# Performance work log

Measured on AMD Instinct MI355X. Metric: run time of the kernel, lower is better.

The kernel has to match this reference:

```python
import jax, jax.numpy as jnp
import numpy as np

N = 50000      # nodes
E = 800000     # edges
C = 128        # in channels
H = 128        # hidden1 = hidden2 = hidden3
B = 256        # graphs in batch
CLS = 10       # classes
MLP_H = 64
EPS = 1e-5


def _lin_params(key, fan_in, fan_out):
    k1, k2 = jax.random.split(key)
    s = 1.0 / np.sqrt(fan_in)
    W = jax.random.uniform(k1, (fan_in, fan_out), jnp.float32, -s, s)
    b = jax.random.uniform(k2, (fan_out,), jnp.float32, -s, s)
    return W, b


def setup_inputs() -> dict:
    key = jax.random.key(0)
    ks = jax.random.split(key, 10)
    x = jax.random.normal(ks[0], (N, C), jnp.float32)
    edge_index = jax.random.randint(ks[1], (2, E), 0, N)
    edge_attr = jax.random.uniform(ks[2], (E,), jnp.float32)
    batch = jnp.sort(jax.random.randint(ks[3], (N,), 0, B))
    W1, b1 = _lin_params(ks[4], C, H)
    W2, b2 = _lin_params(ks[5], H, H)
    W3, b3 = _lin_params(ks[6], H, H)
    gamma = jnp.ones((H,), jnp.float32)
    beta = jnp.zeros((H,), jnp.float32)
    Wm1, bm1 = _lin_params(ks[7], H, MLP_H)
    Wm2, bm2 = _lin_params(ks[8], MLP_H, CLS)
    return dict(x=x, edge_index=edge_index, edge_attr=edge_attr, batch=batch,
                W1=W1, b1=b1, W2=W2, b2=b2, W3=W3, b3=b3,
                gamma=gamma, beta=beta, Wm1=Wm1, bm1=bm1, Wm2=Wm2, bm2=bm2)


def gcn_conv(x, src, dst, ew, W, b):
    # PyG GCNConv: linear (no bias) -> gcn_norm with self-loops -> scatter-add -> +bias
    h = x @ W                                                  # [N, out]
    deg = jax.ops.segment_sum(ew, dst, num_segments=N) + 1.0   # self-loop weight 1
    dinv = jnp.where(deg > 0, jax.lax.rsqrt(deg), 0.0)
    norm = dinv[src] * ew * dinv[dst]                          # [E]
    agg = jax.ops.segment_sum(norm[:, None] * h[src], dst, num_segments=N)
    agg = agg + h * (dinv * dinv)[:, None]                     # self-loop messages
    return agg + b


def reference(x, edge_index, edge_attr, batch,
              W1, b1, W2, b2, W3, b3, gamma, beta, Wm1, bm1, Wm2, bm2):
    src, dst = edge_index[0], edge_index[1]
    ew = edge_attr.reshape(-1)
    h = jax.nn.relu(gcn_conv(x, src, dst, ew, W1, b1))
    h = jax.nn.relu(gcn_conv(h, src, dst, ew, W2, b2))
    h = jax.nn.relu(gcn_conv(h, src, dst, ew, W3, b3))
    # BatchNorm (training-mode batch stats, biased variance)
    mu = jnp.mean(h, axis=0)
    var = jnp.mean((h - mu) ** 2, axis=0)
    h = (h - mu) * jax.lax.rsqrt(var + EPS) * gamma + beta
    # global_mean_pool over graph ids
    counts = jax.ops.segment_sum(jnp.ones((N,), jnp.float32), batch, num_segments=B)
    g = jax.ops.segment_sum(h, batch, num_segments=B) / jnp.maximum(counts, 1.0)[:, None]
    # MLP head (two stacked linears, no activation between)
    pred = (g @ Wm1 + bm1) @ Wm2 + bm2
    return pred
```

## Files before the change

kernel.cpp:

```cpp
#include <hip/hip_runtime.h>
#include <hip/hip_bf16.h>

#define NN 50000
#define EE 800000
#define HH 128
#define BB 256
#define CLS 10
#define MLPH 64
#define CAP 64

#define NBUK 782
#define EPB 10240
#define NBLK_BIN 79
#define SCAN_N (NBUK * NBLK_BIN)
#define SCAN_BLKS 242

typedef __attribute__((ext_vector_type(8))) short short8;
typedef __attribute__((ext_vector_type(4))) float floatx4;

__device__ __forceinline__ float bflo(unsigned u){ unsigned v = u << 16; return __builtin_bit_cast(float, v); }
__device__ __forceinline__ float bfhi(unsigned u){ unsigned v = u & 0xffff0000u; return __builtin_bit_cast(float, v); }
__device__ __forceinline__ unsigned short f2bf(float f){
  unsigned u = __builtin_bit_cast(unsigned, f);
  u += 0x7fffu + ((u >> 16) & 1u);
  return (unsigned short)(u >> 16);
}
__device__ __forceinline__ unsigned pack2(float a, float b){
  return (unsigned)f2bf(a) | ((unsigned)f2bf(b) << 16);
}

__global__ __launch_bounds__(256) void bin_count_k(const int* __restrict__ dst, int* __restrict__ cnts){
  __shared__ int hist[NBUK];
  int t = threadIdx.x, blk = blockIdx.x;
  for (int i = t; i < NBUK; i += 256) hist[i] = 0;
  __syncthreads();
  int e0 = blk * EPB;
  #pragma unroll 4
  for (int i = 0; i < EPB / 256; ++i){
    int e = e0 + i * 256 + t;
    if (e < EE) atomicAdd(&hist[dst[e] >> 6], 1);
  }
  __syncthreads();
  for (int u = t; u < NBUK; u += 256) cnts[u * NBLK_BIN + blk] = hist[u];
}

__global__ __launch_bounds__(256) void scanA_k(int* data, int* bsum){
  __shared__ int sd[256];
  int t = threadIdx.x;
  int i = blockIdx.x * 256 + t;
  int v = (i < SCAN_N) ? data[i] : 0;
  sd[t] = v; __syncthreads();
  for (int off = 1; off < 256; off <<= 1){
    int add = (t >= off) ? sd[t - off] : 0;
    __syncthreads();
    sd[t] += add;
    __syncthreads();
  }
  if (i < SCAN_N) data[i] = sd[t] - v;
  if (t == 255) bsum[blockIdx.x] = sd[255];
}
__global__ __launch_bounds__(256) void scanB_k(int* bsum){
  __shared__ int sd[256];
  int t = threadIdx.x;
  int v = (t < SCAN_BLKS) ? bsum[t] : 0;
  sd[t] = v; __syncthreads();
  for (int off = 1; off < 256; off <<= 1){
    int add = (t >= off) ? sd[t - off] : 0;
    __syncthreads();
    sd[t] += add;
    __syncthreads();
  }
  if (t < SCAN_BLKS) bsum[t] = sd[t] - v;
}
__global__ __launch_bounds__(256) void scanC_k(int* data, const int* bsum){
  int i = blockIdx.x * 256 + threadIdx.x;
  if (i < SCAN_N) data[i] += bsum[i >> 8];
}

__global__ __launch_bounds__(256) void bin_scatter_k(const int* __restrict__ src, const int* __restrict__ dst,
                                                     const float* __restrict__ ew,
                                                     const int* __restrict__ sc, int2* __restrict__ ebin){
  __shared__ int lbase[NBUK];
  __shared__ int lrank[NBUK];
  int t = threadIdx.x, blk = blockIdx.x;
  for (int i = t; i < NBUK; i += 256){ lbase[i] = sc[i * NBLK_BIN + blk]; lrank[i] = 0; }
  __syncthreads();
  int e0 = blk * EPB;
  for (int i = 0; i < EPB / 256; ++i){
    int e = e0 + i * 256 + t;
    if (e < EE){
      int d = dst[e];
      int u = d >> 6;
      int r = atomicAdd(&lrank[u], 1);
      int2 rec; rec.x = src[e] | ((d & 63) << 16); rec.y = __builtin_bit_cast(int, ew[e]);
      ebin[lbase[u] + r] = rec;
    }
  }
}

__global__ __launch_bounds__(256) void bucket_sort_k(const int2* __restrict__ ebin, const int* __restrict__ sc,
                                                     int2* __restrict__ ebuf, int* __restrict__ cnt,
                                                     float* __restrict__ dinv){
  __shared__ int hist[64];
  __shared__ float wsum[64];
  int t = threadIdx.x, u = blockIdx.x;
  if (t < 64){ hist[t] = 0; wsum[t] = 0.0f; }
  __syncthreads();
  int s0 = sc[u * NBLK_BIN];
  int s1 = (u + 1 < NBUK) ? sc[(u + 1) * NBLK_BIN] : EE;
  for (int e = s0 + t; e < s1; e += 256){
    int2 rec = ebin[e];
    int dl = rec.x >> 16;
    int r = atomicAdd(&hist[dl], 1);
    atomicAdd(&wsum[dl], __builtin_bit_cast(float, rec.y));
    if (r < CAP){
      int2 clean; clean.x = rec.x & 0xFFFF; clean.y = rec.y;
      ebuf[((size_t)(u * 64 + dl)) * CAP + r] = clean;
    }
  }
  __syncthreads();
  if (t < 64){
    int n = u * 64 + t;
    if (n < NN){
      cnt[n] = min(hist[t], CAP);
      dinv[n] = rsqrtf(1.0f + wsum[t]);
    }
  }
}

__global__ __launch_bounds__(256) void gbounds_k(const int* __restrict__ batch, int* gstart,
                                                 float* bnsum, float* bnsqs){
  int b = threadIdx.x;
  if (b < HH){ bnsum[b] = 0.0f; bnsqs[b] = 0.0f; }
  int lo = 0, hi = NN;
  while (lo < hi){
    int mid = (lo + hi) >> 1;
    if (batch[mid] < b) lo = mid + 1; else hi = mid;
  }
  gstart[b] = lo;
  if (b == 0) gstart[BB] = NN;
}

__global__ __launch_bounds__(256) void transpose3_k(const float* W1, const float* W2, const float* W3,
                                                    unsigned short* Wt1, unsigned short* Wt2, unsigned short* Wt3){
  int gi = blockIdx.x * 256 + threadIdx.x;
  int w = gi >> 14;
  int i = gi & 16383;
  const float* W = (w == 0) ? W1 : (w == 1) ? W2 : W3;
  unsigned short* Wt = (w == 0) ? Wt1 : (w == 1) ? Wt2 : Wt3;
  int n = i >> 7, k = i & 127;
  Wt[i] = f2bf(W[(k << 7) + n]);
}

__global__ __launch_bounds__(256) void gemm128_k(const unsigned short* __restrict__ X,
                                                 const unsigned short* __restrict__ Wt,
                                                 const float* __restrict__ dinv,
                                                 unsigned short* __restrict__ Gout, int nrows){
  __shared__ __align__(16) unsigned short lw[HH * 136];
  {
    const float4* s4 = (const float4*)Wt;
    float4* d4 = (float4*)lw;
    for (int i = threadIdx.x; i < 2048; i += 256){
      int row = i >> 4, off = i & 15;
      d4[row * 17 + off] = s4[i];
    }
  }
  __syncthreads();
  int wave = threadIdx.x >> 6;
  int lane = threadIdx.x & 63;
  int r16 = lane & 15, quad = lane >> 4;
  int m0 = blockIdx.x * 128 + wave * 32;

  short8 xfrag[2][4];
  float dv[2];
  for (int nt = 0; nt < 2; ++nt){
    int m = m0 + nt * 16 + r16;
    int msafe = (m < nrows) ? m : 0;
    const short8* xrow = (const short8*)(X + (size_t)msafe * HH);
    for (int kk = 0; kk < 4; ++kk) xfrag[nt][kk] = xrow[4 * kk + quad];
    dv[nt] = (m < nrows) ? dinv[m] : 0.0f;
  }
  for (int ct = 0; ct < 8; ++ct){
    floatx4 acc0 = {0.f,0.f,0.f,0.f}, acc1 = {0.f,0.f,0.f,0.f};
    const short8* wrow = (const short8*)(lw + (16 * ct + r16) * 136);
    for (int kk = 0; kk < 4; ++kk){
      short8 wfrag = wrow[4 * kk + quad];
      acc0 = __builtin_amdgcn_mfma_f32_16x16x32_bf16(wfrag, xfrag[0][kk], acc0, 0, 0, 0);
      acc1 = __builtin_amdgcn_mfma_f32_16x16x32_bf16(wfrag, xfrag[1][kk], acc1, 0, 0, 0);
    }
    int ch0 = ct * 16 + quad * 4;
    int m = m0 + r16;
    if (m < nrows){
      uint2 pk; pk.x = pack2(acc0[0] * dv[0], acc0[1] * dv[0]);
      pk.y = pack2(acc0[2] * dv[0], acc0[3] * dv[0]);
      ((uint2*)Gout)[((size_t)m * HH + ch0) >> 2] = pk;
    }
    int m2 = m0 + 16 + r16;
    if (m2 < nrows){
      uint2 pk; pk.x = pack2(acc1[0] * dv[1], acc1[1] * dv[1]);
      pk.y = pack2(acc1[2] * dv[1], acc1[3] * dv[1]);
      ((uint2*)Gout)[((size_t)m2 * HH + ch0) >> 2] = pk;
    }
  }
}

__global__ __launch_bounds__(256) void gemm128_f32_k(const float* __restrict__ X,
                                                     const unsigned short* __restrict__ Wt,
                                                     const float* __restrict__ dinv,
                                                     unsigned short* __restrict__ Gout, int nrows){
  __shared__ __align__(16) unsigned short lw[HH * 136];
  {
    const float4* s4 = (const float4*)Wt;
    float4* d4 = (float4*)lw;
    for (int i = threadIdx.x; i < 2048; i += 256){
      int row = i >> 4, off = i & 15;
      d4[row * 17 + off] = s4[i];
    }
  }
  __syncthreads();
  int wave = threadIdx.x >> 6;
  int lane = threadIdx.x & 63;
  int r16 = lane & 15, quad = lane >> 4;
  int m0 = blockIdx.x * 128 + wave * 32;

  short8 xfrag[2][4];
  float dv[2];
  for (int nt = 0; nt < 2; ++nt){
    int m = m0 + nt * 16 + r16;
    int msafe = (m < nrows) ? m : 0;
    const float4* xr = (const float4*)(X + (size_t)msafe * HH);
    for (int kk = 0; kk < 4; ++kk){
      float4 aA = xr[kk * 8 + quad * 2];
      float4 aB = xr[kk * 8 + quad * 2 + 1];
      uint4 pk;
      pk.x = pack2(aA.x, aA.y); pk.y = pack2(aA.z, aA.w);
      pk.z = pack2(aB.x, aB.y); pk.w = pack2(aB.z, aB.w);
      xfrag[nt][kk] = __builtin_bit_cast(short8, pk);
    }
    dv[nt] = (m < nrows) ? dinv[m] : 0.0f;
  }
  for (int ct = 0; ct < 8; ++ct){
    floatx4 acc0 = {0.f,0.f,0.f,0.f}, acc1 = {0.f,0.f,0.f,0.f};
    const short8* wrow = (const short8*)(lw + (16 * ct + r16) * 136);
    for (int kk = 0; kk < 4; ++kk){
      short8 wfrag = wrow[4 * kk + quad];
      acc0 = __builtin_amdgcn_mfma_f32_16x16x32_bf16(wfrag, xfrag[0][kk], acc0, 0, 0, 0);
      acc1 = __builtin_amdgcn_mfma_f32_16x16x32_bf16(wfrag, xfrag[1][kk], acc1, 0, 0, 0);
    }
    int ch0 = ct * 16 + quad * 4;
    int m = m0 + r16;
    if (m < nrows){
      uint2 pk; pk.x = pack2(acc0[0] * dv[0], acc0[1] * dv[0]);
      pk.y = pack2(acc0[2] * dv[0], acc0[3] * dv[0]);
      ((uint2*)Gout)[((size_t)m * HH + ch0) >> 2] = pk;
    }
    int m2 = m0 + 16 + r16;
    if (m2 < nrows){
      uint2 pk; pk.x = pack2(acc1[0] * dv[1], acc1[1] * dv[1]);
      pk.y = pack2(acc1[2] * dv[1], acc1[3] * dv[1]);
      ((uint2*)Gout)[((size_t)m2 * HH + ch0) >> 2] = pk;
    }
  }
}

__global__ __launch_bounds__(256) void aggregate_k(const unsigned short* __restrict__ Gin,
                                                   const int2* __restrict__ ebuf,
                                                   const int* __restrict__ cnt,
                                                   const float* __restrict__ dinv,
                                                   const float* __restrict__ bias,
                                                   unsigned short* __restrict__ Xout){
  __shared__ float part[4][4][16][8];
  int wv = threadIdx.x >> 6, lane = threadIdx.x & 63;
  int node = blockIdx.x * 4 + wv;
  int g = lane >> 4, l = lane & 15;
  int c = min(cnt[node], CAP);
  int2 rec; rec.x = 0; rec.y = 0;
  if (lane < c) rec = ebuf[(size_t)node * CAP + lane];
  float acc[8] = {0,0,0,0,0,0,0,0};
  const uint4* G4 = (const uint4*)Gin;
  int steps = (c + 3) >> 2;
  #pragma unroll 2
  for (int j = 0; j < steps; ++j){
    int idx = 4 * j + g;
    int sx = __shfl(rec.x, idx);
    float w = __builtin_bit_cast(float, __shfl(rec.y, idx));
    if (idx >= c){ sx = 0; w = 0.0f; }
    uint4 q = G4[(size_t)sx * 16 + l];
    acc[0] = fmaf(w, bflo(q.x), acc[0]);
    acc[1] = fmaf(w, bfhi(q.x), acc[1]);
    acc[2] = fmaf(w, bflo(q.y), acc[2]);
    acc[3] = fmaf(w, bfhi(q.y), acc[3]);
    acc[4] = fmaf(w, bflo(q.z), acc[4]);
    acc[5] = fmaf(w, bfhi(q.z), acc[5]);
    acc[6] = fmaf(w, bflo(q.w), acc[6]);
    acc[7] = fmaf(w, bfhi(q.w), acc[7]);
  }
  #pragma unroll
  for (int k = 0; k < 8; ++k) part[wv][g][l][k] = acc[k];
  __syncthreads();
  int l0 = lane >> 2, k0 = (lane & 3) * 2;
  float a0 = part[wv][0][l0][k0]   + part[wv][1][l0][k0]   + part[wv][2][l0][k0]   + part[wv][3][l0][k0];
  float a1 = part[wv][0][l0][k0+1] + part[wv][1][l0][k0+1] + part[wv][2][l0][k0+1] + part[wv][3][l0][k0+1];
  unsigned gs = ((const unsigned*)Gin)[(size_t)node * 64 + lane];
  a0 += bflo(gs); a1 += bfhi(gs);
  float di = dinv[node];
  float2 bb = ((const float2*)bias)[lane];
  a0 = fmaxf(fmaf(di, a0, bb.x), 0.0f);
  a1 = fmaxf(fmaf(di, a1, bb.y), 0.0f);
  ((unsigned*)Xout)[(size_t)node * 64 + lane] = pack2(a0, a1);
}

__global__ __launch_bounds__(256) void pool_k(const unsigned short* __restrict__ H3,
                                              const int* __restrict__ gstart,
                                              float* __restrict__ S, float* bnsum, float* bnsqs,
                                              float* cntf){
  __shared__ float rs0[256], rs1[256], rq0[256], rq1[256];
  int b = blockIdx.x;
  int t = threadIdx.x, colc = t & 63, sub = t >> 6;
  int start = gstart[b], end = gstart[b + 1];
  const unsigned* Hrow = (const unsigned*)H3;
  float s0 = 0, s1 = 0, q0 = 0, q1 = 0;
  #pragma unroll 4
  for (int n = start + sub; n < end; n += 4){
    unsigned h = Hrow[(size_t)n * 64 + colc];
    float a = bflo(h), c = bfhi(h);
    s0 += a; s1 += c; q0 += a * a; q1 += c * c;
  }
  rs0[t] = s0; rs1[t] = s1; rq0[t] = q0; rq1[t] = q1;
  __syncthreads();
  if (sub == 0){
    float t0 = rs0[colc] + rs0[colc + 64] + rs0[colc + 128] + rs0[colc + 192];
    float t1 = rs1[colc] + rs1[colc + 64] + rs1[colc + 128] + rs1[colc + 192];
    float u0 = rq0[colc] + rq0[colc + 64] + rq0[colc + 128] + rq0[colc + 192];
    float u1 = rq1[colc] + rq1[colc + 64] + rq1[colc + 128] + rq1[colc + 192];
    S[b * HH + 2 * colc]     = t0;
    S[b * HH + 2 * colc + 1] = t1;
    atomicAdd(&bnsum[2 * colc], t0);
    atomicAdd(&bnsum[2 * colc + 1], t1);
    atomicAdd(&bnsqs[2 * colc], u0);
    atomicAdd(&bnsqs[2 * colc + 1], u1);
    if (t == 0) cntf[b] = (float)(end - start);
  }
}

__global__ __launch_bounds__(64) void mlp_head_k(const float* __restrict__ S, const float* __restrict__ cntf,
                                                 const float* __restrict__ bnsum, const float* __restrict__ bnsqs,
                                                 const float* gamma, const float* beta,
                                                 const float* Wm1, const float* bm1,
                                                 const float* Wm2, const float* bm2,
                                                 float* out){
  __shared__ float gb[HH];
  __shared__ float t[MLPH];
  int b = blockIdx.x, j = threadIdx.x;
  float inv = 1.0f / fmaxf(cntf[b], 1.0f);
  for (int c = j; c < HH; c += 64){
    float mu = bnsum[c] * (1.0f / NN);
    float var = bnsqs[c] * (1.0f / NN) - mu * mu;
    float istd = rsqrtf(var + 1e-5f);
    float g = S[b * HH + c] * inv;
    gb[c] = (g - mu) * istd * gamma[c] + beta[c];
  }
  __syncthreads();
  float acc = bm1[j];
  for (int k = 0; k < HH; ++k) acc = fmaf(gb[k], Wm1[k * MLPH + j], acc);
  t[j] = acc;
  __syncthreads();
  if (j < CLS){
    float o = bm2[j];
    for (int k = 0; k < MLPH; ++k) o = fmaf(t[k], Wm2[k * CLS + j], o);
    out[b * CLS + j] = o;
  }
}

static inline size_t al(size_t x){ return (x + 255) & ~(size_t)255; }

extern "C" void kernel_launch(void* const* d_in, const int* in_sizes, int n_in,
                              void* d_out, int out_size, void* d_ws, size_t ws_size,
                              hipStream_t stream){
  const float* x     = (const float*)d_in[0];
  const int*   ei    = (const int*)d_in[1];
  const float* ea    = (const float*)d_in[2];
  const int*   batch = (const int*)d_in[3];
  const float* W1 = (const float*)d_in[4];
  const float* b1 = (const float*)d_in[5];
  const float* W2 = (const float*)d_in[6];
  const float* b2 = (const float*)d_in[7];
  const float* W3 = (const float*)d_in[8];
  const float* b3 = (const float*)d_in[9];
  const float* gamma = (const float*)d_in[10];
  const float* beta  = (const float*)d_in[11];
  const float* Wm1 = (const float*)d_in[12];
  const float* bm1 = (const float*)d_in[13];
  const float* Wm2 = (const float*)d_in[14];
  const float* bm2 = (const float*)d_in[15];
  const int* srcv = ei;
  const int* dstv = ei + EE;

  char* p = (char*)d_ws;
  float* dinv   = (float*)p;            p += al(NN * 4);
  int*   cnt    = (int*)p;              p += al(NN * 4);
  int*   cnts   = (int*)p;              p += al((size_t)SCAN_N * 4);
  int*   bsum   = (int*)p;              p += al(SCAN_BLKS * 4);
  int*   gstart = (int*)p;              p += al((BB + 1) * 4);
  int2*  ebin   = (int2*)p;             p += al((size_t)EE * 8);
  int2*  ebuf   = (int2*)p;             p += al((size_t)NN * CAP * 8);
  unsigned short* Wt1  = (unsigned short*)p; p += al(HH * HH * 2);
  unsigned short* Wt2  = (unsigned short*)p; p += al(HH * HH * 2);
  unsigned short* Wt3  = (unsigned short*)p; p += al(HH * HH * 2);
  unsigned short* bufA = (unsigned short*)p; p += al((size_t)NN * HH * 2);
  unsigned short* bufB = (unsigned short*)p; p += al((size_t)NN * HH * 2);
  float* S     = (float*)p;             p += al(BB * HH * 4);
  float* bnsum = (float*)p;             p += al(HH * 4);
  float* bnsqs = (float*)p;             p += al(HH * 4);
  float* cntf  = (float*)p;             p += al(BB * 4);

  const int nT = 256;
  dim3 gW((NN + 3) / 4);

  bin_count_k<<<dim3(NBLK_BIN), nT, 0, stream>>>(dstv, cnts);
  scanA_k<<<dim3(SCAN_BLKS), nT, 0, stream>>>(cnts, bsum);
  scanB_k<<<dim3(1), nT, 0, stream>>>(bsum);
  scanC_k<<<dim3(SCAN_BLKS), nT, 0, stream>>>(cnts, bsum);
  bin_scatter_k<<<dim3(NBLK_BIN), nT, 0, stream>>>(srcv, dstv, ea, cnts, ebin);
  bucket_sort_k<<<dim3(NBUK), nT, 0, stream>>>(ebin, cnts, ebuf, cnt, dinv);
  gbounds_k<<<dim3(1), nT, 0, stream>>>(batch, gstart, bnsum, bnsqs);
  transpose3_k<<<dim3(192), nT, 0, stream>>>(W1, W2, W3, Wt1, Wt2, Wt3);

  dim3 gGemm((NN + 127) / 128);
  gemm128_f32_k<<<gGemm, nT, 0, stream>>>(x, Wt1, dinv, bufA, NN);
  aggregate_k<<<gW, nT, 0, stream>>>(bufA, ebuf, cnt, dinv, b1, bufB);
  gemm128_k<<<gGemm, nT, 0, stream>>>(bufB, Wt2, dinv, bufA, NN);
  aggregate_k<<<gW, nT, 0, stream>>>(bufA, ebuf, cnt, dinv, b2, bufB);
  gemm128_k<<<gGemm, nT, 0, stream>>>(bufB, Wt3, dinv, bufA, NN);
  aggregate_k<<<gW, nT, 0, stream>>>(bufA, ebuf, cnt, dinv, b3, bufB);

  pool_k<<<dim3(BB), nT, 0, stream>>>(bufB, gstart, S, bnsum, bnsqs, cntf);
  mlp_head_k<<<dim3(BB), dim3(64), 0, stream>>>(S, cntf, bnsum, bnsqs, gamma, beta,
                                                Wm1, bm1, Wm2, bm2, (float*)d_out);
}
```

Baseline: 321.8 us.

## Pack edge records to 4 bytes, widen buckets to 256 nodes, fold scan offsets

Each edge record in the per-node buffer is packed into 32 bits: a 16-bit source index plus a bf16 edge weight. This halves the edge traffic that aggregation reads in all three layers. The bucket binning now uses 256-node buckets with 250 blocks, and the scanC kernel is dropped by adding the block sums directly where the offsets are consumed. The aggregation unroll rises to 4. Edge weights lose precision to bf16, and the 16-bit source field assumes node ids below 65536.

```diff
diff --git a/kernel.cpp b/kernel.cpp
--- a/kernel.cpp
+++ b/kernel.cpp
@@ -9,11 +9,11 @@
 #define MLPH 64
 #define CAP 64
 
-#define NBUK 782
-#define EPB 10240
-#define NBLK_BIN 79
-#define SCAN_N (NBUK * NBLK_BIN)
-#define SCAN_BLKS 242
+#define NBUK 196
+#define NBLK 250
+#define EPB 3200
+#define SCAN_N (NBUK * NBLK)
+#define SCAN_BLKS 192
 
 typedef __attribute__((ext_vector_type(8))) short short8;
 typedef __attribute__((ext_vector_type(4))) float floatx4;
@@ -32,16 +32,14 @@
 __global__ __launch_bounds__(256) void bin_count_k(const int* __restrict__ dst, int* __restrict__ cnts){
   __shared__ int hist[NBUK];
   int t = threadIdx.x, blk = blockIdx.x;
-  for (int i = t; i < NBUK; i += 256) hist[i] = 0;
+  if (t < NBUK) hist[t] = 0;
   __syncthreads();
   int e0 = blk * EPB;
   #pragma unroll 4
-  for (int i = 0; i < EPB / 256; ++i){
-    int e = e0 + i * 256 + t;
-    if (e < EE) atomicAdd(&hist[dst[e] >> 6], 1);
-  }
-  __syncthreads();
-  for (int u = t; u < NBUK; u += 256) cnts[u * NBLK_BIN + blk] = hist[u];
+  for (int i = 0; i < 12; ++i) atomicAdd(&hist[dst[e0 + i * 256 + t] >> 8], 1);
+  if (t < 128) atomicAdd(&hist[dst[e0 + 3072 + t] >> 8], 1);
+  __syncthreads();
+  if (t < NBUK) cnts[t * NBLK + blk] = hist[t];
 }
 
 __global__ __launch_bounds__(256) void scanA_k(int* data, int* bsum){
@@ -72,59 +70,63 @@
   }
   if (t < SCAN_BLKS) bsum[t] = sd[t] - v;
 }
-__global__ __launch_bounds__(256) void scanC_k(int* data, const int* bsum){
-  int i = blockIdx.x * 256 + threadIdx.x;
-  if (i < SCAN_N) data[i] += bsum[i >> 8];
-}
 
 __global__ __launch_bounds__(256) void bin_scatter_k(const int* __restrict__ src, const int* __restrict__ dst,
                                                      const float* __restrict__ ew,
-                                                     const int* __restrict__ sc, int2* __restrict__ ebin){
+                                                     const int* __restrict__ sc, const int* __restrict__ bsum,
+                                                     int2* __restrict__ ebin){
   __shared__ int lbase[NBUK];
   __shared__ int lrank[NBUK];
   int t = threadIdx.x, blk = blockIdx.x;
-  for (int i = t; i < NBUK; i += 256){ lbase[i] = sc[i * NBLK_BIN + blk]; lrank[i] = 0; }
+  if (t < NBUK){
+    int idx = t * NBLK + blk;
+    lbase[t] = sc[idx] + bsum[idx >> 8];
+    lrank[t] = 0;
+  }
   __syncthreads();
   int e0 = blk * EPB;
-  for (int i = 0; i < EPB / 256; ++i){
-    int e = e0 + i * 256 + t;
-    if (e < EE){
+  for (int i = 0; i < 13; ++i){
+    int off = i * 256 + t;
+    if (off < EPB){
+      int e = e0 + off;
       int d = dst[e];
-      int u = d >> 6;
+      int u = d >> 8;
       int r = atomicAdd(&lrank[u], 1);
-      int2 rec; rec.x = src[e] | ((d & 63) << 16); rec.y = __builtin_bit_cast(int, ew[e]);
+      int2 rec; rec.x = src[e] | ((d & 255) << 16); rec.y = __builtin_bit_cast(int, ew[e]);
       ebin[lbase[u] + r] = rec;
     }
   }
 }
 
 __global__ __launch_bounds__(256) void bucket_sort_k(const int2* __restrict__ ebin, const int* __restrict__ sc,
-                                                     int2* __restrict__ ebuf, int* __restrict__ cnt,
+                                                     const int* __restrict__ bsum,
+                                                     unsigned* __restrict__ ebuf, int* __restrict__ cnt,
                                                      float* __restrict__ dinv){
-  __shared__ int hist[64];
-  __shared__ float wsum[64];
+  __shared__ int hist[256];
+  __shared__ float wsum[256];
   int t = threadIdx.x, u = blockIdx.x;
-  if (t < 64){ hist[t] = 0; wsum[t] = 0.0f; }
-  __syncthreads();
-  int s0 = sc[u * NBLK_BIN];
-  int s1 = (u + 1 < NBUK) ? sc[(u + 1) * NBLK_BIN] : EE;
+  hist[t] = 0; wsum[t] = 0.0f;
+  __syncthreads();
+  int i0 = u * NBLK;
+  int s0 = sc[i0] + bsum[i0 >> 8];
+  int s1 = EE;
+  if (u + 1 < NBUK){ int i1 = (u + 1) * NBLK; s1 = sc[i1] + bsum[i1 >> 8]; }
   for (int e = s0 + t; e < s1; e += 256){
     int2 rec = ebin[e];
     int dl = rec.x >> 16;
+    float w = __builtin_bit_cast(float, rec.y);
     int r = atomicAdd(&hist[dl], 1);
-    atomicAdd(&wsum[dl], __builtin_bit_cast(float, rec.y));
+    atomicAdd(&wsum[dl], w);
     if (r < CAP){
-      int2 clean; clean.x = rec.x & 0xFFFF; clean.y = rec.y;
-      ebuf[((size_t)(u * 64 + dl)) * CAP + r] = clean;
-    }
-  }
-  __syncthreads();
-  if (t < 64){
-    int n = u * 64 + t;
-    if (n < NN){
-      cnt[n] = min(hist[t], CAP);
-      dinv[n] = rsqrtf(1.0f + wsum[t]);
-    }
+      unsigned c4 = (unsigned)(rec.x & 0xFFFF) | ((unsigned)f2bf(w) << 16);
+      ebuf[((size_t)(u * 256 + dl)) * CAP + r] = c4;
+    }
+  }
+  __syncthreads();
+  int n = u * 256 + t;
+  if (n < NN){
+    cnt[n] = min(hist[t], CAP);
+    dinv[n] = rsqrtf(1.0f + wsum[t]);
   }
 }
 
@@ -264,7 +266,7 @@
 }
 
 __global__ __launch_bounds__(256) void aggregate_k(const unsigned short* __restrict__ Gin,
-                                                   const int2* __restrict__ ebuf,
+                                                   const unsigned* __restrict__ ebuf,
                                                    const int* __restrict__ cnt,
                                                    const float* __restrict__ dinv,
                                                    const float* __restrict__ bias,
@@ -274,16 +276,17 @@
   int node = blockIdx.x * 4 + wv;
   int g = lane >> 4, l = lane & 15;
   int c = min(cnt[node], CAP);
-  int2 rec; rec.x = 0; rec.y = 0;
+  unsigned rec = 0;
   if (lane < c) rec = ebuf[(size_t)node * CAP + lane];
   float acc[8] = {0,0,0,0,0,0,0,0};
   const uint4* G4 = (const uint4*)Gin;
   int steps = (c + 3) >> 2;
-  #pragma unroll 2
+  #pragma unroll 4
   for (int j = 0; j < steps; ++j){
     int idx = 4 * j + g;
-    int sx = __shfl(rec.x, idx);
-    float w = __builtin_bit_cast(float, __shfl(rec.y, idx));
+    unsigned r = (unsigned)__shfl((int)rec, idx);
+    int sx = r & 0xFFFF;
+    float w = bfhi(r);
     if (idx >= c){ sx = 0; w = 0.0f; }
     uint4 q = G4[(size_t)sx * 16 + l];
     acc[0] = fmaf(w, bflo(q.x), acc[0]);
@@ -403,7 +406,7 @@
   int*   bsum   = (int*)p;              p += al(SCAN_BLKS * 4);
   int*   gstart = (int*)p;              p += al((BB + 1) * 4);
   int2*  ebin   = (int2*)p;             p += al((size_t)EE * 8);
-  int2*  ebuf   = (int2*)p;             p += al((size_t)NN * CAP * 8);
+  unsigned* ebuf = (unsigned*)p;        p += al((size_t)NN * CAP * 4);
   unsigned short* Wt1  = (unsigned short*)p; p += al(HH * HH * 2);
   unsigned short* Wt2  = (unsigned short*)p; p += al(HH * HH * 2);
   unsigned short* Wt3  = (unsigned short*)p; p += al(HH * HH * 2);
@@ -417,12 +420,11 @@
   const int nT = 256;
   dim3 gW((NN + 3) / 4);
 
-  bin_count_k<<<dim3(NBLK_BIN), nT, 0, stream>>>(dstv, cnts);
+  bin_count_k<<<dim3(NBLK), nT, 0, stream>>>(dstv, cnts);
   scanA_k<<<dim3(SCAN_BLKS), nT, 0, stream>>>(cnts, bsum);
   scanB_k<<<dim3(1), nT, 0, stream>>>(bsum);
-  scanC_k<<<dim3(SCAN_BLKS), nT, 0, stream>>>(cnts, bsum);
-  bin_scatter_k<<<dim3(NBLK_BIN), nT, 0, stream>>>(srcv, dstv, ea, cnts, ebin);
-  bucket_sort_k<<<dim3(NBUK), nT, 0, stream>>>(ebin, cnts, ebuf, cnt, dinv);
+  bin_scatter_k<<<dim3(NBLK), nT, 0, stream>>>(srcv, dstv, ea, cnts, bsum, ebin);
+  bucket_sort_k<<<dim3(NBUK), nT, 0, stream>>>(ebin, cnts, bsum, ebuf, cnt, dinv);
   gbounds_k<<<dim3(1), nT, 0, stream>>>(batch, gstart, bnsum, bnsqs);
   transpose3_k<<<dim3(192), nT, 0, stream>>>(W1, W2, W3, Wt1, Wt2, Wt3);
 
```

Result: faster. 286.9 us (-10.9%).
